# Kernel optimization log

Measured on AMD Instinct MI355X. Metric: run time of the kernel, lower is better.

The kernel has to match this reference:

```python
import jax, jax.numpy as jnp
import numpy as np

H, C = 4, 32            # heads, hidden_channel
HC = H * C              # 128
IN = 128                # in_channel
N = 50000               # nodes in sampled subgraph
E = 200000              # edges
USER, ITEM = 50000, 50000
UB = 200                # ubias_num == ibias_num
DIST = 501
BATCH = 1024
NEG = 0.2               # leaky_relu negative slope


def setup_inputs() -> dict:
    key = jax.random.key(0)
    keys = iter(jax.random.split(key, 64))

    def nrm(shape):
        return jax.random.normal(next(keys), shape, dtype=jnp.float32) * 0.05

    def ri(shape, hi):
        return jax.random.randint(next(keys), shape, 0, hi, dtype=jnp.int32)

    inp = {
        # int (graph) inputs
        "node_idx": ri((N,), USER + ITEM + 1),
        "edge_index": ri((2, E), N),
        "edge_type": ri((E,), 6),
        "t_offset_0": ri((E,), UB + 2),
        "t_offset_1": ri((E,), UB + 2),
        "dists_0": ri((E,), DIST),
        "dists_1": ri((E,), DIST),
        "center_nid": ri((BATCH,), N),
        # parameters
        "id_emb": nrm((USER + ITEM + 1, IN)),
        "ucenter_att_bias": nrm((UB + 2, HC)),
        "icenter_att_bias": nrm((UB + 2, HC)),
        "trans_att_bias": nrm((UB + 2, HC)),
        "ucenter_emb_bias": nrm((UB + 2, HC)),
        "icenter_emb_bias": nrm((UB + 2, HC)),
        "trans_emb_bias": nrm((UB + 2, HC)),
        "ucenter_att_bias_2": nrm((UB * 4 + 2, HC)),
        "icenter_att_bias_2": nrm((UB * 4 + 2, HC)),
        "trans_att_bias_2": nrm((UB * 4 + 2, HC)),
        "ucenter_emb_bias_2": nrm((UB * 4 + 2, HC)),
        "icenter_emb_bias_2": nrm((UB * 4 + 2, HC)),
        "trans_emb_bias_2": nrm((UB * 4 + 2, HC)),
        "udist_att_bias": nrm((DIST, HC)),
        "idist_att_bias": nrm((DIST, HC)),
        "udist_emb_bias": nrm((DIST, HC)),
        "idist_emb_bias": nrm((DIST, HC)),
        "udist_att_bias_2": nrm((DIST, HC)),
        "idist_att_bias_2": nrm((DIST, HC)),
        "udist_emb_bias_2": nrm((DIST, HC)),
        "idist_emb_bias_2": nrm((DIST, HC)),
        "trans_head": nrm((IN, HC)),
        "rnn_w": nrm((2 * HC, HC)),           # rnn_update Linear (no bias)
        "w1": nrm((HC * 2 + IN, HC)),          # pred_head layer 1
        "b1": jnp.zeros((HC,), jnp.float32),
        "w2": nrm((HC, ITEM)),                 # pred_head layer 2
        "b2": jnp.zeros((ITEM,), jnp.float32),
        # per-layer conv params (src/dst projections + attention vectors)
        "wl0": nrm((IN, HC)), "wr0": nrm((IN, HC)),
        "asrc0": nrm((H, C)), "adst0": nrm((H, C)),
        "wl1": nrm((HC, HC)), "wr1": nrm((HC, HC)),
        "asrc1": nrm((H, C)), "adst1": nrm((H, C)),
    }
    return inp


def reference(node_idx, edge_index, edge_type, t_offset_0, t_offset_1, dists_0,
              dists_1, center_nid, id_emb, ucenter_att_bias, icenter_att_bias,
              trans_att_bias, ucenter_emb_bias, icenter_emb_bias, trans_emb_bias,
              ucenter_att_bias_2, icenter_att_bias_2, trans_att_bias_2,
              ucenter_emb_bias_2, icenter_emb_bias_2, trans_emb_bias_2,
              udist_att_bias, idist_att_bias, udist_emb_bias, idist_emb_bias,
              udist_att_bias_2, idist_att_bias_2, udist_emb_bias_2,
              idist_emb_bias_2, trans_head, rnn_w, w1, b1, w2, b2,
              wl0, wr0, asrc0, adst0, wl1, wr1, asrc1, adst1):
    x = id_emb[node_idx]                       # [N, IN] gather
    src, dst = edge_index[0], edge_index[1]
    is_u = (edge_type == 0)[:, None]           # user-center homo edges
    is_homo = (edge_type < 2)[:, None]
    involved = ((edge_type == 0) | (edge_type == 2) | (edge_type == 3))[:, None]

    def edge_bias(u_tab, i_tab, tr_tab, toff):
        # homo edges: type-0 -> user table, type-1 -> item table; hetero -> trans table
        b = jnp.where(is_u, u_tab[toff], jnp.where(is_homo, i_tab[toff], tr_tab[toff]))
        return b.reshape(-1, H, C)

    def dist_bias(u_tab, i_tab, dists):
        b = jnp.where(is_u, u_tab[dists], i_tab[dists]) * involved
        return b.reshape(-1, H, C)

    att_b = [edge_bias(ucenter_att_bias, icenter_att_bias, trans_att_bias, t_offset_0),
             edge_bias(ucenter_att_bias_2, icenter_att_bias_2, trans_att_bias_2, t_offset_1)]
    emb_b = [edge_bias(ucenter_emb_bias, icenter_emb_bias, trans_emb_bias, t_offset_0),
             edge_bias(ucenter_emb_bias_2, icenter_emb_bias_2, trans_emb_bias_2, t_offset_1)]
    att_d = [dist_bias(udist_att_bias, idist_att_bias, dists_0),
             dist_bias(udist_att_bias_2, idist_att_bias_2, dists_1)]
    emb_d = [dist_bias(udist_emb_bias, idist_emb_bias, dists_0),
             dist_bias(udist_emb_bias_2, idist_emb_bias_2, dists_1)]

    n_nodes = x.shape[0]

    def conv(h, wl, wr, asrc, adst, ab, eb, ad, ed):
        k = (h @ wl).reshape(n_nodes, H, C)
        q = (h @ wr).reshape(n_nodes, H, C)
        msg = k[src] + eb + ed                                   # [E,H,C]
        logit = jax.nn.leaky_relu(
            jnp.einsum('ehc,hc->eh', k[src] + ab + ad, asrc)
            + jnp.einsum('ehc,hc->eh', q[dst], adst), NEG)        # [E,H]
        m = jax.ops.segment_max(logit, dst, num_segments=n_nodes)
        a = jnp.exp(logit - m[dst])
        den = jax.ops.segment_sum(a, dst, num_segments=n_nodes)
        alpha = a / jnp.maximum(den[dst], 1e-16)
        out = jax.ops.segment_sum(alpha[..., None] * msg, dst, num_segments=n_nodes)
        return out.reshape(n_nodes, HC)

    layers = [(wl0, wr0, asrc0, adst0), (wl1, wr1, asrc1, adst1)]
    x_inter = [x]
    cur = x
    for i in range(2):
        last = cur @ trans_head if i == 0 else cur
        wl, wr, asrc, adst = layers[i]
        cur = conv(cur, wl, wr, asrc, adst, att_b[i], emb_b[i], att_d[i], emb_d[i])
        cur = jnp.tanh(jnp.concatenate([cur, last], axis=-1) @ rnn_w)
        x_inter.append(cur)
        if i != 1:
            cur = jax.nn.relu(cur)   # dropout: eval mode -> identity

    feat = jnp.concatenate(x_inter, axis=-1)[center_nid]   # [B, 2*HC+IN]
    hdd = jax.nn.leaky_relu(feat @ w1 + b1, NEG)            # dropout eval -> identity
    logits = hdd @ w2 + b2                                  # [B, ITEM]
    return logits
```

## Files before the change

kernel.cpp:

```cpp
#include <hip/hip_runtime.h>
#include <cstdint>
#include <cstddef>

typedef unsigned short u16;
typedef __attribute__((ext_vector_type(8))) short short8;
typedef __attribute__((ext_vector_type(4))) float f32x4;
typedef __attribute__((ext_vector_type(4))) int i32x4;

#define HC_ 128
#define CAP 32
#define OFF_U0   0
#define OFF_I0   202
#define OFF_T0   404
#define OFF_UD0  606
#define OFF_ID0  1107
#define OFF_U2   1608
#define OFF_I2   2410
#define OFF_T2   3212
#define OFF_UD2  4014
#define OFF_ID2  4515
#define DOT_ROWS 5016

__device__ __forceinline__ float b2f(u16 u) {
  union { unsigned int i; float f; } v; v.i = ((unsigned int)u) << 16; return v.f;
}
__device__ __forceinline__ u16 f2b(float f) {
  union { float f; unsigned int i; } v; v.f = f;
  unsigned int r = v.i + 0x7fffu + ((v.i >> 16) & 1u);
  return (u16)(r >> 16);
}

__global__ __launch_bounds__(256) void prolog_k(
    const int* __restrict__ nidx, const float* __restrict__ emb, u16* __restrict__ x,
    const float* u0, const float* i0, const float* t0, const float* ud0, const float* id0,
    const float* u2, const float* i2, const float* t2, const float* ud2, const float* id2,
    const float* __restrict__ asrc0, const float* __restrict__ asrc1,
    float* __restrict__ dots,
    const float* __restrict__ wr0, const float* __restrict__ adst0,
    const float* __restrict__ wr1, const float* __restrict__ adst1,
    float* __restrict__ wq,
    const float* __restrict__ rnn_w, u16* __restrict__ rnn_wb,
    const float* __restrict__ th, u16* __restrict__ Wt,
    int* __restrict__ cur, float* __restrict__ kdot0, float* __restrict__ kdot1, int Nn)
{
  int b = blockIdx.x, t = threadIdx.x;
  const int nbCur  = (Nn + 255) >> 8;
  const int nbKd   = (Nn * 4 + 255) >> 8;
  const int nbGx   = (Nn * 16 + 255) >> 8;
  const int nbDots = (DOT_ROWS * 4 + 255) >> 8;

  if (b < nbCur) { int i = b * 256 + t; if (i < Nn) cur[i] = 0; return; }
  b -= nbCur;
  if (b < nbKd) {
    int i = b * 256 + t;
    if (i < Nn * 4) { kdot0[i] = 0.f; kdot1[i] = 0.f; }
    return;
  }
  b -= nbKd;
  if (b < nbGx) {
    int i = b * 256 + t;
    int n = i >> 4, c = (i & 15) << 3;
    if (n < Nn) {
      int id = nidx[n];
      const float* s = emb + (size_t)id * HC_ + c;
      u16 tmp[8];
#pragma unroll
      for (int j = 0; j < 8; ++j) tmp[j] = f2b(s[j]);
      *(short8*)(x + (size_t)n * HC_ + c) = *(short8*)tmp;
    }
    return;
  }
  b -= nbGx;
  if (b < nbDots) {
    int i = b * 256 + t;
    if (i < DOT_ROWS * 4) {
      int r = i >> 2, h = i & 3;
      const float* tab; int lr; const float* as;
      if      (r < OFF_I0)  { tab = u0;  lr = r;            as = asrc0; }
      else if (r < OFF_T0)  { tab = i0;  lr = r - OFF_I0;   as = asrc0; }
      else if (r < OFF_UD0) { tab = t0;  lr = r - OFF_T0;   as = asrc0; }
      else if (r < OFF_ID0) { tab = ud0; lr = r - OFF_UD0;  as = asrc0; }
      else if (r < OFF_U2)  { tab = id0; lr = r - OFF_ID0;  as = asrc0; }
      else if (r < OFF_I2)  { tab = u2;  lr = r - OFF_U2;   as = asrc1; }
      else if (r < OFF_T2)  { tab = i2;  lr = r - OFF_I2;   as = asrc1; }
      else if (r < OFF_UD2) { tab = t2;  lr = r - OFF_T2;   as = asrc1; }
      else if (r < OFF_ID2) { tab = ud2; lr = r - OFF_UD2;  as = asrc1; }
      else                  { tab = id2; lr = r - OFF_ID2;  as = asrc1; }
      float s = 0.f;
#pragma unroll
      for (int c = 0; c < 32; ++c)
        s += tab[(size_t)lr * HC_ + h * 32 + c] * as[h * 32 + c];
      dots[i] = s;
    }
    return;
  }
  b -= nbDots;
  if (b < 4) {
    int i = b * 256 + t;
    int layer = i >> 9, k = (i >> 2) & 127, h = i & 3;
    const float* wr = layer ? wr1 : wr0;
    const float* ad = layer ? adst1 : adst0;
    float s = 0.f;
#pragma unroll
    for (int c = 0; c < 32; ++c)
      s += wr[(size_t)k * HC_ + h * 32 + c] * ad[h * 32 + c];
    wq[i] = s;
    return;
  }
  b -= 4;
  if (b < 128) {
    int i = b * 256 + t;
    rnn_wb[i] = f2b(rnn_w[i]);
    return;
  }
  b -= 128;
  {
    int i = b * 256 + t;
    if (i < 16384) {
      int r = i >> 7, c = i & 127;
      float s = 0.f;
#pragma unroll 8
      for (int k = 0; k < 128; ++k)
        s += th[r * 128 + k] * rnn_w[(size_t)(128 + k) * 128 + c];
      Wt[i] = f2b(s);
    }
  }
}

__global__ void fill_k(const int* __restrict__ src, const int* __restrict__ dst,
                       const int* __restrict__ ety,
                       const int* __restrict__ toff0, const int* __restrict__ toff1,
                       const int* __restrict__ dist0, const int* __restrict__ dist1,
                       const float* __restrict__ dots,
                       int* __restrict__ cur, i32x4* __restrict__ bkt, int E)
{
  int e = blockIdx.x * blockDim.x + threadIdx.x;
  if (e >= E) return;
  int d = dst[e];
  int slot = atomicAdd(&cur[d], 1);
  if (slot >= CAP) return;
  int s = src[e], ty = ety[e];
  int to0 = toff0[e], to1 = toff1[e], di0 = dist0[e], di1 = dist1[e];
  bool inv = (ty == 0 || ty == 2 || ty == 3);
  int ar0 = (ty == 0) ? (OFF_U0 + to0) : (ty < 2) ? (OFF_I0 + to0) : (OFF_T0 + to0);
  int ar1 = (ty == 0) ? (OFF_U2 + to1) : (ty < 2) ? (OFF_I2 + to1) : (OFF_T2 + to1);
  f32x4 e0 = *(const f32x4*)(dots + (size_t)ar0 * 4);
  f32x4 e1 = *(const f32x4*)(dots + (size_t)ar1 * 4);
  if (inv) {
    int dr0 = ((ty == 0) ? OFF_UD0 : OFF_ID0) + di0;
    int dr1 = ((ty == 0) ? OFF_UD2 : OFF_ID2) + di1;
    e0 += *(const f32x4*)(dots + (size_t)dr0 * 4);
    e1 += *(const f32x4*)(dots + (size_t)dr1 * 4);
  }
  size_t base = ((size_t)d * CAP + slot) * 4;
  i32x4 p0; p0[0] = s; p0[1] = ty; p0[2] = to0; p0[3] = di0;
  i32x4 p1; p1[0] = s; p1[1] = ty; p1[2] = to1; p1[3] = di1;
  f32x4* fb = (f32x4*)bkt;
  bkt[base + 0] = p0;
  fb [base + 1] = e0;
  bkt[base + 2] = p1;
  fb [base + 3] = e1;
}

template<int EPI, int RELUA, int KS, int AF32, int OF32, int KQ>
__global__ __launch_bounds__(256) void gemm_k(
    const void* __restrict__ A_, const float* __restrict__ W,
    const float* __restrict__ bias, void* __restrict__ C_,
    const float* __restrict__ asrc, const float* __restrict__ wqt,
    float* __restrict__ kdot, float* __restrict__ qdot, int M, int N)
{
  const int lane = threadIdx.x & 63;
  const int wave = threadIdx.x >> 6;
  const int quad = lane >> 4;
  const int l16  = lane & 15;
  const int n0   = blockIdx.y * 64 + wave * 16;
  if (n0 >= N) return;

  short8 bfrag[KS];
#pragma unroll
  for (int ks = 0; ks < KS; ++ks) {
    short8 bf;
    const int kb = ks * 32 + quad * 8;
#pragma unroll
    for (int j = 0; j < 8; ++j)
      bf[j] = (short)f2b(W[(size_t)(kb + j) * N + n0 + l16]);
    bfrag[ks] = bf;
  }
  float bv = 0.f;
  if (EPI == 2 || EPI == 3) bv = bias[n0 + l16];

  const int mtiles = M >> 4;
  for (int mt = blockIdx.x; mt < mtiles; mt += gridDim.x) {
    f32x4 acc = {0.f, 0.f, 0.f, 0.f};
    float qp[4] = {0.f, 0.f, 0.f, 0.f};
    if (AF32) {
      const float* arow = (const float*)A_ + (size_t)(mt * 16 + l16) * (KS * 32);
#pragma unroll
      for (int ks = 0; ks < KS; ++ks) {
        short8 af;
#pragma unroll
        for (int j = 0; j < 8; ++j) {
          float v = arow[ks * 32 + quad * 8 + j];
          if (RELUA) v = fmaxf(v, 0.f);
          af[j] = (short)f2b(v);
        }
        acc = __builtin_amdgcn_mfma_f32_16x16x32_bf16(af, bfrag[ks], acc, 0, 0, 0);
      }
    } else {
      const u16* arow = (const u16*)A_ + (size_t)(mt * 16 + l16) * (KS * 32);
#pragma unroll
      for (int ks = 0; ks < KS; ++ks) {
        short8 af = *(const short8*)(arow + ks * 32 + quad * 8);
        if (RELUA) {
#pragma unroll
          for (int j = 0; j < 8; ++j) af[j] = (af[j] < (short)0) ? (short)0 : af[j];
        }
        if (KQ) {
#pragma unroll
          for (int j = 0; j < 8; ++j) {
            float v = b2f((u16)af[j]);
            const float* wr = wqt + (size_t)(ks * 32 + quad * 8 + j) * 4;
            qp[0] += v * wr[0]; qp[1] += v * wr[1];
            qp[2] += v * wr[2]; qp[3] += v * wr[3];
          }
        }
        acc = __builtin_amdgcn_mfma_f32_16x16x32_bf16(af, bfrag[ks], acc, 0, 0, 0);
      }
    }

    if (KQ) {
#pragma unroll
      for (int h = 0; h < 4; ++h) {
        qp[h] += __shfl_xor(qp[h], 16, 64);
        qp[h] += __shfl_xor(qp[h], 32, 64);
      }
      if (blockIdx.y == 0 && quad == 0) {
        f32x4 qv; qv[0] = qp[0]; qv[1] = qp[1]; qv[2] = qp[2]; qv[3] = qp[3];
        *(f32x4*)(qdot + (size_t)(mt * 16 + l16) * 4) = qv;
      }
      const int hh = n0 >> 5;
      const float asv = asrc[n0 + l16];
#pragma unroll
      for (int r = 0; r < 4; ++r) {
        float sr = acc[r] * asv;
        sr += __shfl_xor(sr, 1, 64); sr += __shfl_xor(sr, 2, 64);
        sr += __shfl_xor(sr, 4, 64); sr += __shfl_xor(sr, 8, 64);
        if (l16 == 0)
          atomicAdd(&kdot[(size_t)(mt * 16 + quad * 4 + r) * 4 + hh], sr);
      }
    }

#pragma unroll
    for (int r = 0; r < 4; ++r) {
      float v = acc[r];
      if (EPI == 2)      { v += bv; v = (v > 0.f) ? v : 0.2f * v; }
      else if (EPI == 3) { v += bv; }
      const size_t idx = (size_t)(mt * 16 + quad * 4 + r) * N + n0 + l16;
      if (OF32) ((float*)C_)[idx] = v;
      else      ((u16*)C_)[idx] = f2b(v);
    }
  }
}

template<int RELU2, int GATHER>
__global__ __launch_bounds__(256) void gemm2_k(
    const float* __restrict__ A1, const u16* __restrict__ W1,
    const u16* __restrict__ A2, const u16* __restrict__ W2,
    const int* __restrict__ gidx, u16* __restrict__ Cout, int M)
{
  const int lane = threadIdx.x & 63;
  const int wave = threadIdx.x >> 6;
  const int quad = lane >> 4;
  const int l16  = lane & 15;
  const int n0   = blockIdx.y * 64 + wave * 16;

  short8 bf1[4], bf2[4];
#pragma unroll
  for (int ks = 0; ks < 4; ++ks) {
    short8 a, b;
    const int kb = ks * 32 + quad * 8;
#pragma unroll
    for (int j = 0; j < 8; ++j) {
      a[j] = (short)W1[(size_t)(kb + j) * HC_ + n0 + l16];
      b[j] = (short)W2[(size_t)(kb + j) * HC_ + n0 + l16];
    }
    bf1[ks] = a; bf2[ks] = b;
  }

  const int mtiles = M >> 4;
  for (int mt = blockIdx.x; mt < mtiles; mt += gridDim.x) {
    const int rowm = mt * 16 + l16;
    const int g = GATHER ? gidx[rowm] : rowm;
    const float* a1 = A1 + (size_t)g * HC_;
    const u16*   a2 = A2 + (size_t)g * HC_;
    f32x4 acc = {0.f, 0.f, 0.f, 0.f};
#pragma unroll
    for (int ks = 0; ks < 4; ++ks) {
      short8 af;
      const float* p = a1 + ks * 32 + quad * 8;
#pragma unroll
      for (int j = 0; j < 8; ++j) af[j] = (short)f2b(p[j]);
      acc = __builtin_amdgcn_mfma_f32_16x16x32_bf16(af, bf1[ks], acc, 0, 0, 0);
    }
#pragma unroll
    for (int ks = 0; ks < 4; ++ks) {
      short8 af = *(const short8*)(a2 + ks * 32 + quad * 8);
      if (RELU2) {
#pragma unroll
        for (int j = 0; j < 8; ++j) af[j] = (af[j] < (short)0) ? (short)0 : af[j];
      }
      acc = __builtin_amdgcn_mfma_f32_16x16x32_bf16(af, bf2[ks], acc, 0, 0, 0);
    }
#pragma unroll
    for (int r = 0; r < 4; ++r)
      Cout[(size_t)(mt * 16 + quad * 4 + r) * HC_ + n0 + l16] = f2b(tanhf(acc[r]));
  }
}

__global__ __launch_bounds__(256) void gemm_feat_k(
    const u16* __restrict__ x, const u16* __restrict__ h1, const u16* __restrict__ h2c,
    const int* __restrict__ center, const float* __restrict__ W,
    const float* __restrict__ bias, u16* __restrict__ C, int M, int N)
{
  const int lane = threadIdx.x & 63;
  const int wave = threadIdx.x >> 6;
  const int quad = lane >> 4;
  const int l16  = lane & 15;
  const int n0   = blockIdx.y * 64 + wave * 16;

  short8 bfrag[12];
#pragma unroll
  for (int ks = 0; ks < 12; ++ks) {
    short8 bf;
    const int kb = ks * 32 + quad * 8;
#pragma unroll
    for (int j = 0; j < 8; ++j)
      bf[j] = (short)f2b(W[(size_t)(kb + j) * N + n0 + l16]);
    bfrag[ks] = bf;
  }
  const float bv = bias[n0 + l16];

  const int mtiles = M >> 4;
  for (int mt = blockIdx.x; mt < mtiles; mt += gridDim.x) {
    const int rowm = mt * 16 + l16;
    const int nid = center[rowm];
    f32x4 acc = {0.f, 0.f, 0.f, 0.f};
#pragma unroll
    for (int ks = 0; ks < 12; ++ks) {
      const u16* p;
      if (ks < 4)      p = x   + (size_t)nid  * HC_ + ks * 32;
      else if (ks < 8) p = h1  + (size_t)nid  * HC_ + (ks - 4) * 32;
      else             p = h2c + (size_t)rowm * HC_ + (ks - 8) * 32;
      short8 af = *(const short8*)(p + quad * 8);
      acc = __builtin_amdgcn_mfma_f32_16x16x32_bf16(af, bfrag[ks], acc, 0, 0, 0);
    }
#pragma unroll
    for (int r = 0; r < 4; ++r) {
      float v = acc[r] + bv;
      v = (v > 0.f) ? v : 0.2f * v;
      C[(size_t)(mt * 16 + quad * 4 + r) * HC_ + n0 + l16] = f2b(v);
    }
  }
}

template<int MASKED>
__global__ __launch_bounds__(256) void conv_k(
    const int* __restrict__ cur, const i32x4* __restrict__ bkt, int layerOff,
    const u16* __restrict__ kbuf,
    const float* __restrict__ kdot, const float* __restrict__ qdot,
    const float* __restrict__ uemb, const float* __restrict__ iemb,
    const float* __restrict__ temb,
    const float* __restrict__ udemb, const float* __restrict__ idemb,
    const int* __restrict__ center, float* __restrict__ CO, int Ncnt)
{
  int wid = (blockIdx.x * blockDim.x + threadIdx.x) >> 6;
  if (wid >= Ncnt) return;
  const int lane = threadIdx.x & 63;
  const int n = MASKED ? center[wid] : wid;
  int cnt = cur[n]; if (cnt > CAP) cnt = CAP;
  const int h0 = lane >> 5;
  const int h1 = h0 + 2;
  const float q0 = qdot[n * 4 + h0];
  const float q1 = qdot[n * 4 + h1];
  const i32x4* base = bkt + (size_t)n * CAP * 4 + layerOff;
  const f32x4* fbase = (const f32x4*)base;

  float den0 = 0.f, den1 = 0.f;
  for (int e = 0; e < cnt; ++e) {
    i32x4 p = base[e * 4];
    f32x4 ed = fbase[e * 4 + 1];
    int s = p[0];
    float l0 = kdot[s * 4 + h0] + q0 + ed[h0];
    float l1 = kdot[s * 4 + h1] + q1 + ed[h1];
    l0 = (l0 > 0.f) ? l0 : 0.2f * l0;
    l1 = (l1 > 0.f) ? l1 : 0.2f * l1;
    den0 += __expf(fminf(l0, 30.f));
    den1 += __expf(fminf(l1, 30.f));
  }
  const float r0 = 1.f / fmaxf(den0, 1e-16f);
  const float r1 = 1.f / fmaxf(den1, 1e-16f);

  float acc0 = 0.f, acc1 = 0.f;
  for (int e = 0; e < cnt; ++e) {
    i32x4 p = base[e * 4];
    f32x4 ed = fbase[e * 4 + 1];
    int s = p[0], ty = p[1], to = p[2], di = p[3];
    float l0 = kdot[s * 4 + h0] + q0 + ed[h0];
    float l1 = kdot[s * 4 + h1] + q1 + ed[h1];
    l0 = (l0 > 0.f) ? l0 : 0.2f * l0;
    l1 = (l1 > 0.f) ? l1 : 0.2f * l1;
    float al0 = __expf(fminf(l0, 30.f)) * r0;
    float al1 = __expf(fminf(l1, 30.f)) * r1;

    float m0 = b2f(kbuf[(size_t)s * HC_ + lane]);
    float m1 = b2f(kbuf[(size_t)s * HC_ + 64 + lane]);
    const float* et = (ty == 0) ? uemb : (ty < 2) ? iemb : temb;
    m0 += et[(size_t)to * HC_ + lane];
    m1 += et[(size_t)to * HC_ + 64 + lane];
    if (ty == 0 || ty == 2 || ty == 3) {
      const float* dt = (ty == 0) ? udemb : idemb;
      m0 += dt[(size_t)di * HC_ + lane];
      m1 += dt[(size_t)di * HC_ + 64 + lane];
    }
    acc0 += al0 * m0;
    acc1 += al1 * m1;
  }
  CO[(size_t)n * HC_ + lane]      = acc0;
  CO[(size_t)n * HC_ + 64 + lane] = acc1;
}

extern "C" void kernel_launch(void* const* d_in, const int* in_sizes, int n_in,
                              void* d_out, int out_size, void* d_ws, size_t ws_size,
                              hipStream_t stream)
{
  (void)n_in; (void)out_size; (void)ws_size;
  const int* node_idx = (const int*)d_in[0];
  const int* eidx     = (const int*)d_in[1];
  const int* etype    = (const int*)d_in[2];
  const int* toff0    = (const int*)d_in[3];
  const int* toff1    = (const int*)d_in[4];
  const int* dist0    = (const int*)d_in[5];
  const int* dist1    = (const int*)d_in[6];
  const int* center   = (const int*)d_in[7];
  const float* id_emb   = (const float*)d_in[8];
  const float* u_att    = (const float*)d_in[9];
  const float* i_att    = (const float*)d_in[10];
  const float* t_att    = (const float*)d_in[11];
  const float* u_emb    = (const float*)d_in[12];
  const float* i_emb    = (const float*)d_in[13];
  const float* t_emb    = (const float*)d_in[14];
  const float* u_att2   = (const float*)d_in[15];
  const float* i_att2   = (const float*)d_in[16];
  const float* t_att2   = (const float*)d_in[17];
  const float* u_emb2   = (const float*)d_in[18];
  const float* i_emb2   = (const float*)d_in[19];
  const float* t_emb2   = (const float*)d_in[20];
  const float* ud_att   = (const float*)d_in[21];
  const float* id_att   = (const float*)d_in[22];
  const float* ud_emb   = (const float*)d_in[23];
  const float* id_embd  = (const float*)d_in[24];
  const float* ud_att2  = (const float*)d_in[25];
  const float* id_att2  = (const float*)d_in[26];
  const float* ud_emb2  = (const float*)d_in[27];
  const float* id_emb2  = (const float*)d_in[28];
  const float* trans_head = (const float*)d_in[29];
  const float* rnn_w    = (const float*)d_in[30];
  const float* w1       = (const float*)d_in[31];
  const float* b1       = (const float*)d_in[32];
  const float* w2       = (const float*)d_in[33];
  const float* b2       = (const float*)d_in[34];
  const float* wl0      = (const float*)d_in[35];
  const float* wr0      = (const float*)d_in[36];
  const float* asrc0    = (const float*)d_in[37];
  const float* adst0    = (const float*)d_in[38];
  const float* wl1      = (const float*)d_in[39];
  const float* wr1      = (const float*)d_in[40];
  const float* asrc1    = (const float*)d_in[41];
  const float* adst1    = (const float*)d_in[42];

  const int N_    = in_sizes[0];
  const int E_    = in_sizes[2];
  const int B_    = in_sizes[7];
  const int ITEM_ = in_sizes[34];
  const int* esrc = eidx;
  const int* edst = eidx + E_;

  char* ws = (char*)d_ws;
  size_t off = 0;
  auto alloc = [&](size_t bytes) -> char* {
    char* p = ws + off;
    off += (bytes + 255) & ~(size_t)255;
    return p;
  };
  float* CO_b  = (float*)alloc((size_t)N_ * HC_ * 4);
  u16*   k_b   = (u16*)  alloc((size_t)N_ * HC_ * 2);
  u16*   x_b   = (u16*)  alloc((size_t)N_ * HC_ * 2);
  u16*   h1_b  = (u16*)  alloc((size_t)N_ * HC_ * 2);
  float* kdot0 = (float*)alloc((size_t)N_ * 4 * 4);
  float* kdot1 = (float*)alloc((size_t)N_ * 4 * 4);
  float* qdot  = (float*)alloc((size_t)N_ * 4 * 4);
  float* dots  = (float*)alloc((size_t)DOT_ROWS * 4 * 4);
  float* wq    = (float*)alloc(1024 * 4);
  u16*   rnn_wb= (u16*)  alloc(256 * HC_ * 2);
  u16*   Wt    = (u16*)  alloc(HC_ * HC_ * 2);
  u16*   h2c   = (u16*)  alloc((size_t)B_ * HC_ * 2);
  u16*   hdd   = (u16*)  alloc((size_t)B_ * HC_ * 2);
  int*   cur   = (int*)  alloc((size_t)N_ * 4);
  i32x4* bkt   = (i32x4*)alloc((size_t)N_ * CAP * 64);

  const int TB = 256;
  auto nb = [&](long long t) { return (int)((t + TB - 1) / TB); };

  const int nbCur  = (N_ + 255) / 256;
  const int nbKd   = (N_ * 4 + 255) / 256;
  const int nbGx   = (N_ * 16 + 255) / 256;
  const int nbDots = (DOT_ROWS * 4 + 255) / 256;
  const int prologBlocks = nbCur + nbKd + nbGx + nbDots + 4 + 128 + 64;
  prolog_k<<<prologBlocks, TB, 0, stream>>>(
      node_idx, id_emb, x_b,
      u_att, i_att, t_att, ud_att, id_att,
      u_att2, i_att2, t_att2, ud_att2, id_att2,
      asrc0, asrc1, dots,
      wr0, adst0, wr1, adst1, wq,
      rnn_w, rnn_wb, trans_head, Wt,
      cur, kdot0, kdot1, N_);

  fill_k<<<nb(E_), TB, 0, stream>>>(esrc, edst, etype, toff0, toff1, dist0, dist1,
                                    dots, cur, bkt, E_);

  gemm_k<0,0,4,0,0,1><<<dim3(640, 2), TB, 0, stream>>>(
      x_b, wl0, nullptr, k_b, asrc0, wq, kdot0, qdot, N_, HC_);

  conv_k<0><<<nb((long long)N_ * 64), TB, 0, stream>>>(
      cur, bkt, 0, k_b, kdot0, qdot,
      u_emb, i_emb, t_emb, ud_emb, id_embd, nullptr, CO_b, N_);

  gemm2_k<0,0><<<dim3(640, 2), TB, 0, stream>>>(CO_b, rnn_wb, x_b, Wt, nullptr, h1_b, N_);

  gemm_k<0,1,4,0,0,1><<<dim3(640, 2), TB, 0, stream>>>(
      h1_b, wl1, nullptr, k_b, asrc1, wq + 512, kdot1, qdot, N_, HC_);

  conv_k<1><<<nb((long long)B_ * 64), TB, 0, stream>>>(
      cur, bkt, 2, k_b, kdot1, qdot,
      u_emb2, i_emb2, t_emb2, ud_emb2, id_emb2, center, CO_b, B_);

  gemm2_k<1,1><<<dim3(64, 2), TB, 0, stream>>>(CO_b, rnn_wb, h1_b, rnn_wb + HC_ * HC_,
                                               center, h2c, B_);

  gemm_feat_k<<<dim3(64, 2), TB, 0, stream>>>(x_b, h1_b, h2c, center, w1, b1, hdd, B_, HC_);

  gemm_k<3,0,4,0,1,0><<<dim3(4, (ITEM_ + 63) / 64), TB, 0, stream>>>(
      hdd, w2, b2, d_out, nullptr, nullptr, nullptr, nullptr, B_, ITEM_);
}
```

Baseline: 665.3 us.

## Split edge buckets into packed SoA, cache softmax exps, fuse tail GEMMs

Edge buckets are stored as separate packed metadata and edge-dot arrays per layer, shrinking the records read in the conv loops. The conv kernel stores the per-edge exponentials in shared memory, so the second pass skips recomputing logits and reloading kdot. The center-node RNN GEMM and the pred-head first layer are fused into one kernel that keeps h2 in LDS. The final output GEMM uses one block per column tile looping over all rows, trading parallelism for weight-fragment reuse.

```diff
diff --git a/kernel.cpp b/kernel.cpp
--- a/kernel.cpp
+++ b/kernel.cpp
@@ -5,7 +5,6 @@
 typedef unsigned short u16;
 typedef __attribute__((ext_vector_type(8))) short short8;
 typedef __attribute__((ext_vector_type(4))) float f32x4;
-typedef __attribute__((ext_vector_type(4))) int i32x4;
 
 #define HC_ 128
 #define CAP 32
@@ -132,7 +131,9 @@
                        const int* __restrict__ toff0, const int* __restrict__ toff1,
                        const int* __restrict__ dist0, const int* __restrict__ dist1,
                        const float* __restrict__ dots,
-                       int* __restrict__ cur, i32x4* __restrict__ bkt, int E)
+                       int* __restrict__ cur,
+                       int2* __restrict__ m0a, f32x4* __restrict__ e0a,
+                       int2* __restrict__ m1a, f32x4* __restrict__ e1a, int E)
 {
   int e = blockIdx.x * blockDim.x + threadIdx.x;
   if (e >= E) return;
@@ -152,14 +153,11 @@
     e0 += *(const f32x4*)(dots + (size_t)dr0 * 4);
     e1 += *(const f32x4*)(dots + (size_t)dr1 * 4);
   }
-  size_t base = ((size_t)d * CAP + slot) * 4;
-  i32x4 p0; p0[0] = s; p0[1] = ty; p0[2] = to0; p0[3] = di0;
-  i32x4 p1; p1[0] = s; p1[1] = ty; p1[2] = to1; p1[3] = di1;
-  f32x4* fb = (f32x4*)bkt;
-  bkt[base + 0] = p0;
-  fb [base + 1] = e0;
-  bkt[base + 2] = p1;
-  fb [base + 3] = e1;
+  size_t ix = (size_t)d * CAP + slot;
+  m0a[ix] = make_int2(s, ty | (to0 << 3) | (di0 << 13));
+  m1a[ix] = make_int2(s, ty | (to1 << 3) | (di1 << 13));
+  e0a[ix] = e0;
+  e1a[ix] = e1;
 }
 
 template<int EPI, int RELUA, int KS, int AF32, int OF32, int KQ>
@@ -262,11 +260,10 @@
   }
 }
 
-template<int RELU2, int GATHER>
 __global__ __launch_bounds__(256) void gemm2_k(
     const float* __restrict__ A1, const u16* __restrict__ W1,
     const u16* __restrict__ A2, const u16* __restrict__ W2,
-    const int* __restrict__ gidx, u16* __restrict__ Cout, int M)
+    u16* __restrict__ Cout, int M)
 {
   const int lane = threadIdx.x & 63;
   const int wave = threadIdx.x >> 6;
@@ -290,9 +287,8 @@
   const int mtiles = M >> 4;
   for (int mt = blockIdx.x; mt < mtiles; mt += gridDim.x) {
     const int rowm = mt * 16 + l16;
-    const int g = GATHER ? gidx[rowm] : rowm;
-    const float* a1 = A1 + (size_t)g * HC_;
-    const u16*   a2 = A2 + (size_t)g * HC_;
+    const float* a1 = A1 + (size_t)rowm * HC_;
+    const u16*   a2 = A2 + (size_t)rowm * HC_;
     f32x4 acc = {0.f, 0.f, 0.f, 0.f};
 #pragma unroll
     for (int ks = 0; ks < 4; ++ks) {
@@ -305,10 +301,6 @@
 #pragma unroll
     for (int ks = 0; ks < 4; ++ks) {
       short8 af = *(const short8*)(a2 + ks * 32 + quad * 8);
-      if (RELU2) {
-#pragma unroll
-        for (int j = 0; j < 8; ++j) af[j] = (af[j] < (short)0) ? (short)0 : af[j];
-      }
       acc = __builtin_amdgcn_mfma_f32_16x16x32_bf16(af, bf2[ks], acc, 0, 0, 0);
     }
 #pragma unroll
@@ -317,55 +309,10 @@
   }
 }
 
-__global__ __launch_bounds__(256) void gemm_feat_k(
-    const u16* __restrict__ x, const u16* __restrict__ h1, const u16* __restrict__ h2c,
-    const int* __restrict__ center, const float* __restrict__ W,
-    const float* __restrict__ bias, u16* __restrict__ C, int M, int N)
-{
-  const int lane = threadIdx.x & 63;
-  const int wave = threadIdx.x >> 6;
-  const int quad = lane >> 4;
-  const int l16  = lane & 15;
-  const int n0   = blockIdx.y * 64 + wave * 16;
-
-  short8 bfrag[12];
-#pragma unroll
-  for (int ks = 0; ks < 12; ++ks) {
-    short8 bf;
-    const int kb = ks * 32 + quad * 8;
-#pragma unroll
-    for (int j = 0; j < 8; ++j)
-      bf[j] = (short)f2b(W[(size_t)(kb + j) * N + n0 + l16]);
-    bfrag[ks] = bf;
-  }
-  const float bv = bias[n0 + l16];
-
-  const int mtiles = M >> 4;
-  for (int mt = blockIdx.x; mt < mtiles; mt += gridDim.x) {
-    const int rowm = mt * 16 + l16;
-    const int nid = center[rowm];
-    f32x4 acc = {0.f, 0.f, 0.f, 0.f};
-#pragma unroll
-    for (int ks = 0; ks < 12; ++ks) {
-      const u16* p;
-      if (ks < 4)      p = x   + (size_t)nid  * HC_ + ks * 32;
-      else if (ks < 8) p = h1  + (size_t)nid  * HC_ + (ks - 4) * 32;
-      else             p = h2c + (size_t)rowm * HC_ + (ks - 8) * 32;
-      short8 af = *(const short8*)(p + quad * 8);
-      acc = __builtin_amdgcn_mfma_f32_16x16x32_bf16(af, bfrag[ks], acc, 0, 0, 0);
-    }
-#pragma unroll
-    for (int r = 0; r < 4; ++r) {
-      float v = acc[r] + bv;
-      v = (v > 0.f) ? v : 0.2f * v;
-      C[(size_t)(mt * 16 + quad * 4 + r) * HC_ + n0 + l16] = f2b(v);
-    }
-  }
-}
-
 template<int MASKED>
 __global__ __launch_bounds__(256) void conv_k(
-    const int* __restrict__ cur, const i32x4* __restrict__ bkt, int layerOff,
+    const int* __restrict__ cur, const int2* __restrict__ meta,
+    const f32x4* __restrict__ edot,
     const u16* __restrict__ kbuf,
     const float* __restrict__ kdot, const float* __restrict__ qdot,
     const float* __restrict__ uemb, const float* __restrict__ iemb,
@@ -373,6 +320,8 @@
     const float* __restrict__ udemb, const float* __restrict__ idemb,
     const int* __restrict__ center, float* __restrict__ CO, int Ncnt)
 {
+  __shared__ float als[4][CAP][4];
+  const int wv = threadIdx.x >> 6;
   int wid = (blockIdx.x * blockDim.x + threadIdx.x) >> 6;
   if (wid >= Ncnt) return;
   const int lane = threadIdx.x & 63;
@@ -382,35 +331,32 @@
   const int h1 = h0 + 2;
   const float q0 = qdot[n * 4 + h0];
   const float q1 = qdot[n * 4 + h1];
-  const i32x4* base = bkt + (size_t)n * CAP * 4 + layerOff;
-  const f32x4* fbase = (const f32x4*)base;
+  const int2* mb = meta + (size_t)n * CAP;
+  const f32x4* eb = edot + (size_t)n * CAP;
 
   float den0 = 0.f, den1 = 0.f;
   for (int e = 0; e < cnt; ++e) {
-    i32x4 p = base[e * 4];
-    f32x4 ed = fbase[e * 4 + 1];
-    int s = p[0];
+    int s = mb[e].x;
+    f32x4 ed = eb[e];
     float l0 = kdot[s * 4 + h0] + q0 + ed[h0];
     float l1 = kdot[s * 4 + h1] + q1 + ed[h1];
     l0 = (l0 > 0.f) ? l0 : 0.2f * l0;
     l1 = (l1 > 0.f) ? l1 : 0.2f * l1;
-    den0 += __expf(fminf(l0, 30.f));
-    den1 += __expf(fminf(l1, 30.f));
+    float a0 = __expf(fminf(l0, 30.f));
+    float a1 = __expf(fminf(l1, 30.f));
+    den0 += a0; den1 += a1;
+    if ((lane & 31) == 0) { als[wv][e][h0] = a0; als[wv][e][h1] = a1; }
   }
   const float r0 = 1.f / fmaxf(den0, 1e-16f);
   const float r1 = 1.f / fmaxf(den1, 1e-16f);
 
   float acc0 = 0.f, acc1 = 0.f;
   for (int e = 0; e < cnt; ++e) {
-    i32x4 p = base[e * 4];
-    f32x4 ed = fbase[e * 4 + 1];
-    int s = p[0], ty = p[1], to = p[2], di = p[3];
-    float l0 = kdot[s * 4 + h0] + q0 + ed[h0];
-    float l1 = kdot[s * 4 + h1] + q1 + ed[h1];
-    l0 = (l0 > 0.f) ? l0 : 0.2f * l0;
-    l1 = (l1 > 0.f) ? l1 : 0.2f * l1;
-    float al0 = __expf(fminf(l0, 30.f)) * r0;
-    float al1 = __expf(fminf(l1, 30.f)) * r1;
+    int2 mrec = mb[e];
+    int s = mrec.x;
+    int ty = mrec.y & 7, to = (mrec.y >> 3) & 1023, di = mrec.y >> 13;
+    float al0 = als[wv][e][h0] * r0;
+    float al1 = als[wv][e][h1] * r1;
 
     float m0 = b2f(kbuf[(size_t)s * HC_ + lane]);
     float m1 = b2f(kbuf[(size_t)s * HC_ + 64 + lane]);
@@ -427,6 +373,95 @@
   }
   CO[(size_t)n * HC_ + lane]      = acc0;
   CO[(size_t)n * HC_ + 64 + lane] = acc1;
+}
+
+__global__ __launch_bounds__(256) void gh_k(
+    const float* __restrict__ CO, const u16* __restrict__ rnn_wb,
+    const u16* __restrict__ h1, const u16* __restrict__ xb,
+    const int* __restrict__ center, const float* __restrict__ w1,
+    const float* __restrict__ b1, u16* __restrict__ hdd)
+{
+  __shared__ u16 h2s[16][136];
+  const int t = threadIdx.x;
+  const int lane = t & 63, wave = t >> 6, quad = lane >> 4, l16 = lane & 15;
+  const int mt = blockIdx.x;
+  const int rowm = mt * 16 + l16;
+  const int nid = center[rowm];
+  const u16* W1 = rnn_wb;
+  const u16* W2 = rnn_wb + HC_ * HC_;
+
+#pragma unroll
+  for (int half = 0; half < 2; ++half) {
+    const int n0 = half * 64 + wave * 16;
+    short8 bf1[4], bf2[4];
+#pragma unroll
+    for (int ks = 0; ks < 4; ++ks) {
+      short8 a, b;
+      const int kb = ks * 32 + quad * 8;
+#pragma unroll
+      for (int j = 0; j < 8; ++j) {
+        a[j] = (short)W1[(size_t)(kb + j) * HC_ + n0 + l16];
+        b[j] = (short)W2[(size_t)(kb + j) * HC_ + n0 + l16];
+      }
+      bf1[ks] = a; bf2[ks] = b;
+    }
+    const float* a1 = CO + (size_t)nid * HC_;
+    const u16*   a2 = h1 + (size_t)nid * HC_;
+    f32x4 acc = {0.f, 0.f, 0.f, 0.f};
+#pragma unroll
+    for (int ks = 0; ks < 4; ++ks) {
+      short8 af;
+      const float* p = a1 + ks * 32 + quad * 8;
+#pragma unroll
+      for (int j = 0; j < 8; ++j) af[j] = (short)f2b(p[j]);
+      acc = __builtin_amdgcn_mfma_f32_16x16x32_bf16(af, bf1[ks], acc, 0, 0, 0);
+    }
+#pragma unroll
+    for (int ks = 0; ks < 4; ++ks) {
+      short8 af = *(const short8*)(a2 + ks * 32 + quad * 8);
+#pragma unroll
+      for (int j = 0; j < 8; ++j) af[j] = (af[j] < (short)0) ? (short)0 : af[j];
+      acc = __builtin_amdgcn_mfma_f32_16x16x32_bf16(af, bf2[ks], acc, 0, 0, 0);
+    }
+#pragma unroll
+    for (int r = 0; r < 4; ++r)
+      h2s[quad * 4 + r][n0 + l16] = f2b(tanhf(acc[r]));
+  }
+  __syncthreads();
+
+#pragma unroll
+  for (int half = 0; half < 2; ++half) {
+    const int n0 = half * 64 + wave * 16;
+    short8 bfrag[12];
+#pragma unroll
+    for (int ks = 0; ks < 12; ++ks) {
+      short8 bf;
+      const int kb = ks * 32 + quad * 8;
+#pragma unroll
+      for (int j = 0; j < 8; ++j)
+        bf[j] = (short)f2b(w1[(size_t)(kb + j) * HC_ + n0 + l16]);
+      bfrag[ks] = bf;
+    }
+    const float bv = b1[n0 + l16];
+    f32x4 acc = {0.f, 0.f, 0.f, 0.f};
+#pragma unroll
+    for (int ks = 0; ks < 12; ++ks) {
+      short8 af;
+      if (ks < 4)
+        af = *(const short8*)(xb + (size_t)nid * HC_ + ks * 32 + quad * 8);
+      else if (ks < 8)
+        af = *(const short8*)(h1 + (size_t)nid * HC_ + (ks - 4) * 32 + quad * 8);
+      else
+        af = *(const short8*)(&h2s[l16][(ks - 8) * 32 + quad * 8]);
+      acc = __builtin_amdgcn_mfma_f32_16x16x32_bf16(af, bfrag[ks], acc, 0, 0, 0);
+    }
+#pragma unroll
+    for (int r = 0; r < 4; ++r) {
+      float v = acc[r] + bv;
+      v = (v > 0.f) ? v : 0.2f * v;
+      hdd[(size_t)(mt * 16 + quad * 4 + r) * HC_ + n0 + l16] = f2b(v);
+    }
+  }
 }
 
 extern "C" void kernel_launch(void* const* d_in, const int* in_sizes, int n_in,
@@ -503,10 +538,12 @@
   float* wq    = (float*)alloc(1024 * 4);
   u16*   rnn_wb= (u16*)  alloc(256 * HC_ * 2);
   u16*   Wt    = (u16*)  alloc(HC_ * HC_ * 2);
-  u16*   h2c   = (u16*)  alloc((size_t)B_ * HC_ * 2);
   u16*   hdd   = (u16*)  alloc((size_t)B_ * HC_ * 2);
   int*   cur   = (int*)  alloc((size_t)N_ * 4);
-  i32x4* bkt   = (i32x4*)alloc((size_t)N_ * CAP * 64);
+  int2*  m0a   = (int2*) alloc((size_t)N_ * CAP * 8);
+  int2*  m1a   = (int2*) alloc((size_t)N_ * CAP * 8);
+  f32x4* e0a   = (f32x4*)alloc((size_t)N_ * CAP * 16);
+  f32x4* e1a   = (f32x4*)alloc((size_t)N_ * CAP * 16);
 
   const int TB = 256;
   auto nb = [&](long long t) { return (int)((t + TB - 1) / TB); };
@@ -526,29 +563,26 @@
       cur, kdot0, kdot1, N_);
 
   fill_k<<<nb(E_), TB, 0, stream>>>(esrc, edst, etype, toff0, toff1, dist0, dist1,
-                                    dots, cur, bkt, E_);
+                                    dots, cur, m0a, e0a, m1a, e1a, E_);
 
   gemm_k<0,0,4,0,0,1><<<dim3(640, 2), TB, 0, stream>>>(
       x_b, wl0, nullptr, k_b, asrc0, wq, kdot0, qdot, N_, HC_);
 
   conv_k<0><<<nb((long long)N_ * 64), TB, 0, stream>>>(
-      cur, bkt, 0, k_b, kdot0, qdot,
+      cur, m0a, e0a, k_b, kdot0, qdot,
       u_emb, i_emb, t_emb, ud_emb, id_embd, nullptr, CO_b, N_);
 
-  gemm2_k<0,0><<<dim3(640, 2), TB, 0, stream>>>(CO_b, rnn_wb, x_b, Wt, nullptr, h1_b, N_);
+  gemm2_k<<<dim3(640, 2), TB, 0, stream>>>(CO_b, rnn_wb, x_b, Wt, h1_b, N_);
 
   gemm_k<0,1,4,0,0,1><<<dim3(640, 2), TB, 0, stream>>>(
       h1_b, wl1, nullptr, k_b, asrc1, wq + 512, kdot1, qdot, N_, HC_);
 
   conv_k<1><<<nb((long long)B_ * 64), TB, 0, stream>>>(
-      cur, bkt, 2, k_b, kdot1, qdot,
+      cur, m1a, e1a, k_b, kdot1, qdot,
       u_emb2, i_emb2, t_emb2, ud_emb2, id_emb2, center, CO_b, B_);
 
-  gemm2_k<1,1><<<dim3(64, 2), TB, 0, stream>>>(CO_b, rnn_wb, h1_b, rnn_wb + HC_ * HC_,
-                                               center, h2c, B_);
-
-  gemm_feat_k<<<dim3(64, 2), TB, 0, stream>>>(x_b, h1_b, h2c, center, w1, b1, hdd, B_, HC_);
-
-  gemm_k<3,0,4,0,1,0><<<dim3(4, (ITEM_ + 63) / 64), TB, 0, stream>>>(
+  gh_k<<<B_ / 16, TB, 0, stream>>>(CO_b, rnn_wb, h1_b, x_b, center, w1, b1, hdd);
+
+  gemm_k<3,0,4,0,1,0><<<dim3(1, (ITEM_ + 63) / 64), TB, 0, stream>>>(
       hdd, w2, b2, d_out, nullptr, nullptr, nullptr, nullptr, B_, ITEM_);
 }
```

Result: slower. 679.7 us (+2.2%).
